# Optimization experiments

Hardware: AMD Instinct MI355X
Metric: run time of the kernel (lower is better)

The kernel has to match this reference:

```python
import jax, jax.numpy as jnp
import numpy as np

# Volume dims: 3 directional stacks, batch 1, 64 channels, (8,16,16) latent volume
STACK, B, C, D, H, W = 3, 1, 64, 8, 16, 16
S = D * H * W  # 2048 attention positions
NUM_HEADS = 8


def setup_inputs() -> dict:
    key = jax.random.key(0)
    kq, kk, kv = jax.random.split(key, 3)
    shape = (STACK, B, C, D, H, W)
    keys = jax.random.normal(kk, shape, dtype=jnp.float32)
    queries = jax.random.normal(kq, shape, dtype=jnp.float32)
    values = jax.random.normal(kv, shape, dtype=jnp.float32)
    # Causal (lower-triangular) mask over flattened spatial positions
    attn_mask = jnp.tril(jnp.ones((S, S), dtype=bool))
    return {"keys": keys, "queries": queries, "values": values,
            "attn_mask": attn_mask, "num_heads": NUM_HEADS}


def reference(keys, queries, values, attn_mask, num_heads):
    s, b, c, d, h, w = keys.shape
    nh = num_heads
    ck = c // nh            # channels per head (attention head dim)
    seq = d * h * w         # spatial positions = attention sequence length
    scale = ck ** (-0.5)
    # (s, b, nh, ck, seq)
    q = queries.reshape(s, b, nh, ck, seq) * scale
    k = keys.reshape(s, b, nh, ck, seq)
    v = values.reshape(s, b, nh, ck, seq)
    # logits[i, j] = <q[:, i], k[:, j]> over channel dim -> (s, b, nh, seq, seq)
    logits = jnp.einsum('sbhci,sbhcj->sbhij', q, k)
    # eval mode: dropout-on-logits trick is training-only, skipped here
    logits = jnp.where(attn_mask, logits, -jnp.inf)
    weights = jax.nn.softmax(logits, axis=-1)
    # (s, b, nh, seq, ck)
    attn = jnp.einsum('sbhij,sbhjc->sbhic', weights, jnp.swapaxes(v, 3, 4))
    # transpose back to channels-first, then restore spatial dims
    out = jnp.swapaxes(attn, 3, 4).reshape(s, b, nh * ck, d, h, w)
    return out
```

## Files before the change

### kernel.cpp

```cpp
#include <hip/hip_runtime.h>
#include <hip/hip_bf16.h>

constexpr int NPROB  = 24;
constexpr int SEQ    = 2048;
constexpr int CK     = 8;
constexpr int NSTRIP = SEQ / 16;

typedef __attribute__((ext_vector_type(8))) short bf16x8;
typedef __attribute__((ext_vector_type(4))) float f32x4;

__device__ constexpr float QSCALE = 0.35355339059327373f * 1.4426950408889634f;

__device__ inline unsigned packbf(float a, float b) {
    float2 t{a, b};
    __hip_bfloat162 h = __float22bfloat162_rn(t);
    unsigned r; __builtin_memcpy(&r, &h, 4); return r;
}

constexpr int T1 = NPROB * SEQ;
constexpr int T2 = NPROB * CK * (SEQ / 8);
constexpr int T3 = NPROB * 8  * (SEQ / 8);

__global__ __launch_bounds__(256) void prepass(
    const float* __restrict__ K, const float* __restrict__ Q,
    const float* __restrict__ V,
    uint4* __restrict__ Qt4, uint4* __restrict__ Kt4, uint4* __restrict__ V164)
{
    const int t = blockIdx.x * 256 + threadIdx.x;
    if (t < T1) {
        const int prob = t >> 11, j = t & (SEQ - 1);
        const float* qs = Q + prob * CK * SEQ + j;
        const float* ks = K + prob * CK * SEQ + j;
        uint4 qo, ko;
        qo.x = packbf(qs[0 * SEQ] * QSCALE, qs[1 * SEQ] * QSCALE);
        qo.y = packbf(qs[2 * SEQ] * QSCALE, qs[3 * SEQ] * QSCALE);
        qo.z = packbf(qs[4 * SEQ] * QSCALE, qs[5 * SEQ] * QSCALE);
        qo.w = packbf(qs[6 * SEQ] * QSCALE, qs[7 * SEQ] * QSCALE);
        ko.x = packbf(ks[0 * SEQ], ks[1 * SEQ]);
        ko.y = packbf(ks[2 * SEQ], ks[3 * SEQ]);
        ko.z = packbf(ks[4 * SEQ], ks[5 * SEQ]);
        ko.w = packbf(ks[6 * SEQ], ks[7 * SEQ]);
        Qt4[t] = qo;
        Kt4[t] = ko;
    } else if (t < T1 + T2) {
        const int idx  = t - T1;
        const int prob = idx >> 11;
        const int rem  = idx & 2047;
        const int c    = rem >> 8;
        const int u    = rem & 255;
        const int c32  = u >> 2;
        const int g    = u & 3;
        const float* vs = V + prob * CK * SEQ + c * SEQ + c32 * 32;
        const float4 a = *reinterpret_cast<const float4*>(vs + 4 * g);
        const float4 b = *reinterpret_cast<const float4*>(vs + 16 + 4 * g);
        uint4 vo;
        vo.x = packbf(a.x, a.y); vo.y = packbf(a.z, a.w);
        vo.z = packbf(b.x, b.y); vo.w = packbf(b.z, b.w);
        V164[prob * 4096 + c32 * 64 + g * 16 + c] = vo;
    } else {
        const int idx  = t - T1 - T2;
        const int prob = idx >> 11;
        const int rem  = idx & 2047;
        const int r    = rem >> 8;
        const int u    = rem & 255;
        const int c32  = u >> 2;
        const int g    = u & 3;
        const unsigned w = (r == 0) ? 0x3F803F80u : 0u;
        V164[prob * 4096 + c32 * 64 + g * 16 + (8 + r)] = uint4{w, w, w, w};
    }
}

__global__ __launch_bounds__(256) void attn_main(
    const uint4* __restrict__ Qt4, const uint4* __restrict__ Kt4,
    const uint4* __restrict__ V164, float* __restrict__ OUT)
{
    const int bid   = blockIdx.x;
    const int prob  = bid % NPROB;
    const int strip = (NSTRIP - 1) - (bid / NPROB);
    const int i0    = strip * 16;
    const int t  = threadIdx.x;
    const int w  = t >> 6;
    const int l  = t & 63;
    const int li = l & 15, g = l >> 4;

    const uint4* Ktp = Kt4 + prob * SEQ;
    const uint4* Vp  = V164 + prob * 4096;

    union { bf16x8 v; uint4 u; } qf;
    qf.u = (g == 0) ? Qt4[prob * SEQ + i0 + li] : uint4{0, 0, 0, 0};

    f32x4 acc = {0.f, 0.f, 0.f, 0.f};
    const f32x4 zc = {0.f, 0.f, 0.f, 0.f};
    const int mconst = li - 4 * g;

    const int NU = i0 >> 5;

#pragma unroll 2
    for (int p = w; p < NU; p += 4) {
        const int j0 = p * 32;
        union { bf16x8 v; uint4 u; } k0, k1, vf;
        k0.u = Ktp[j0 + li];
        k1.u = Ktp[j0 + 16 + li];
        vf.u = Vp[(p << 6) + l];
        f32x4 d0 = __builtin_amdgcn_mfma_f32_16x16x32_bf16(k0.v, qf.v, zc, 0, 0, 0);
        f32x4 d1 = __builtin_amdgcn_mfma_f32_16x16x32_bf16(k1.v, qf.v, zc, 0, 0, 0);
#pragma unroll
        for (int r = 0; r < 4; ++r) { d0[r] = exp2f(d0[r]); d1[r] = exp2f(d1[r]); }
        union { bf16x8 v; unsigned u[4]; } pa;
        pa.u[0] = packbf(d0[0], d0[1]);
        pa.u[1] = packbf(d0[2], d0[3]);
        pa.u[2] = packbf(d1[0], d1[1]);
        pa.u[3] = packbf(d1[2], d1[3]);
        acc = __builtin_amdgcn_mfma_f32_16x16x32_bf16(pa.v, vf.v, acc, 0, 0, 0);
    }

    if ((NU & 3) == w) {
        const int j0 = NU * 32;
        union { bf16x8 v; uint4 u; } k0, k1, vf;
        union { bf16x8 v; unsigned u[4]; } pa;
        vf.u = Vp[(NU << 6) + l];
        if (i0 & 16) {
            k0.u = Ktp[j0 + li];
            k1.u = Ktp[j0 + 16 + li];
            f32x4 d0 = __builtin_amdgcn_mfma_f32_16x16x32_bf16(k0.v, qf.v, zc, 0, 0, 0);
            f32x4 d1 = __builtin_amdgcn_mfma_f32_16x16x32_bf16(k1.v, qf.v, zc, 0, 0, 0);
#pragma unroll
            for (int r = 0; r < 4; ++r) {
                d0[r] = exp2f(d0[r]);
                d1[r] = (r <= mconst) ? exp2f(d1[r]) : 0.f;
            }
            pa.u[0] = packbf(d0[0], d0[1]);
            pa.u[1] = packbf(d0[2], d0[3]);
            pa.u[2] = packbf(d1[0], d1[1]);
            pa.u[3] = packbf(d1[2], d1[3]);
        } else {
            k0.u = Ktp[j0 + li];
            f32x4 d0 = __builtin_amdgcn_mfma_f32_16x16x32_bf16(k0.v, qf.v, zc, 0, 0, 0);
#pragma unroll
            for (int r = 0; r < 4; ++r)
                d0[r] = (r <= mconst) ? exp2f(d0[r]) : 0.f;
            pa.u[0] = packbf(d0[0], d0[1]);
            pa.u[1] = packbf(d0[2], d0[3]);
            pa.u[2] = 0u;
            pa.u[3] = 0u;
        }
        acc = __builtin_amdgcn_mfma_f32_16x16x32_bf16(pa.v, vf.v, acc, 0, 0, 0);
    }

    __shared__ f32x4 lds[4][64];
    lds[w][l] = acc;
    __syncthreads();
    if (w != 0) return;
#pragma unroll
    for (int ww = 1; ww < 4; ++ww) {
        const f32x4 o = lds[ww][l];
#pragma unroll
        for (int r = 0; r < 4; ++r) acc[r] += o[r];
    }

    const int idxR = ((g << 4) + 8) << 2;
    float inv[4];
#pragma unroll
    for (int r = 0; r < 4; ++r) {
        const float rs = __int_as_float(
            __builtin_amdgcn_ds_bpermute(idxR, __float_as_int(acc[r])));
        inv[r] = 1.0f / rs;
    }
    if (li < CK) {
#pragma unroll
        for (int r = 0; r < 4; ++r)
            OUT[(prob * CK + li) * SEQ + i0 + 4 * g + r] = acc[r] * inv[r];
    }
}

extern "C" void kernel_launch(void* const* d_in, const int* in_sizes, int n_in,
                              void* d_out, int out_size, void* d_ws, size_t ws_size,
                              hipStream_t stream) {
    const float* K = (const float*)d_in[0];
    const float* Q = (const float*)d_in[1];
    const float* V = (const float*)d_in[2];
    float* OUT = (float*)d_out;

    uint4* Qt4  = (uint4*)d_ws;
    uint4* Kt4  = (uint4*)((char*)d_ws + 786432);
    uint4* V164 = (uint4*)((char*)d_ws + 1572864);

    prepass<<<dim3((T1 + T2 + T3) / 256), dim3(256), 0, stream>>>(K, Q, V, Qt4, Kt4, V164);
    attn_main<<<dim3(NPROB * NSTRIP), dim3(256), 0, stream>>>(Qt4, Kt4, V164, OUT);
}
```

Before: 91.92 us.

## Process 64-query strips per block and convert Q inside attention kernel

Each block now handles four 16-row query tiles instead of one, so every K and V fragment loaded from global memory feeds four query tiles. The diagonal tile masking is generalized to per-tile thresholds. Q bf16 conversion and scaling moves out of the prepass into the main kernel, which removes a workspace write and read. The cost is fewer blocks (768 instead of 3072), so there is less parallelism and more load imbalance across the causal strips, plus higher register use per thread.

```diff
diff --git a/kernel.cpp b/kernel.cpp
--- a/kernel.cpp
+++ b/kernel.cpp
@@ -1,10 +1,10 @@
 #include <hip/hip_runtime.h>
 #include <hip/hip_bf16.h>
 
-constexpr int NPROB  = 24;
-constexpr int SEQ    = 2048;
-constexpr int CK     = 8;
-constexpr int NSTRIP = SEQ / 16;
+constexpr int NPROB   = 24;
+constexpr int SEQ     = 2048;
+constexpr int CK      = 8;
+constexpr int NSTRIP64 = SEQ / 64;
 
 typedef __attribute__((ext_vector_type(8))) short bf16x8;
 typedef __attribute__((ext_vector_type(4))) float f32x4;
@@ -17,33 +17,26 @@
     unsigned r; __builtin_memcpy(&r, &h, 4); return r;
 }
 
-constexpr int T1 = NPROB * SEQ;
-constexpr int T2 = NPROB * CK * (SEQ / 8);
-constexpr int T3 = NPROB * 8  * (SEQ / 8);
+constexpr int TK = NPROB * SEQ;
+constexpr int TB = NPROB * CK * (SEQ / 8);
+constexpr int TC = NPROB * 8  * (SEQ / 8);
 
 __global__ __launch_bounds__(256) void prepass(
-    const float* __restrict__ K, const float* __restrict__ Q,
-    const float* __restrict__ V,
-    uint4* __restrict__ Qt4, uint4* __restrict__ Kt4, uint4* __restrict__ V164)
+    const float* __restrict__ K, const float* __restrict__ V,
+    uint4* __restrict__ Kt4, uint4* __restrict__ V164)
 {
     const int t = blockIdx.x * 256 + threadIdx.x;
-    if (t < T1) {
+    if (t < TK) {
         const int prob = t >> 11, j = t & (SEQ - 1);
-        const float* qs = Q + prob * CK * SEQ + j;
         const float* ks = K + prob * CK * SEQ + j;
-        uint4 qo, ko;
-        qo.x = packbf(qs[0 * SEQ] * QSCALE, qs[1 * SEQ] * QSCALE);
-        qo.y = packbf(qs[2 * SEQ] * QSCALE, qs[3 * SEQ] * QSCALE);
-        qo.z = packbf(qs[4 * SEQ] * QSCALE, qs[5 * SEQ] * QSCALE);
-        qo.w = packbf(qs[6 * SEQ] * QSCALE, qs[7 * SEQ] * QSCALE);
+        uint4 ko;
         ko.x = packbf(ks[0 * SEQ], ks[1 * SEQ]);
         ko.y = packbf(ks[2 * SEQ], ks[3 * SEQ]);
         ko.z = packbf(ks[4 * SEQ], ks[5 * SEQ]);
         ko.w = packbf(ks[6 * SEQ], ks[7 * SEQ]);
-        Qt4[t] = qo;
         Kt4[t] = ko;
-    } else if (t < T1 + T2) {
-        const int idx  = t - T1;
+    } else if (t < TK + TB) {
+        const int idx  = t - TK;
         const int prob = idx >> 11;
         const int rem  = idx & 2047;
         const int c    = rem >> 8;
@@ -58,7 +51,7 @@
         vo.z = packbf(b.x, b.y); vo.w = packbf(b.z, b.w);
         V164[prob * 4096 + c32 * 64 + g * 16 + c] = vo;
     } else {
-        const int idx  = t - T1 - T2;
+        const int idx  = t - TK - TB;
         const int prob = idx >> 11;
         const int rem  = idx & 2047;
         const int r    = rem >> 8;
@@ -71,13 +64,13 @@
 }
 
 __global__ __launch_bounds__(256) void attn_main(
-    const uint4* __restrict__ Qt4, const uint4* __restrict__ Kt4,
+    const float* __restrict__ Q, const uint4* __restrict__ Kt4,
     const uint4* __restrict__ V164, float* __restrict__ OUT)
 {
-    const int bid   = blockIdx.x;
-    const int prob  = bid % NPROB;
-    const int strip = (NSTRIP - 1) - (bid / NPROB);
-    const int i0    = strip * 16;
+    const int bid  = blockIdx.x;
+    const int prob = bid % NPROB;
+    const int s64  = (NSTRIP64 - 1) - (bid / NPROB);
+    const int i0   = s64 * 64;
     const int t  = threadIdx.x;
     const int w  = t >> 6;
     const int l  = t & 63;
@@ -86,76 +79,81 @@
     const uint4* Ktp = Kt4 + prob * SEQ;
     const uint4* Vp  = V164 + prob * 4096;
 
-    union { bf16x8 v; uint4 u; } qf;
-    qf.u = (g == 0) ? Qt4[prob * SEQ + i0 + li] : uint4{0, 0, 0, 0};
-
-    f32x4 acc = {0.f, 0.f, 0.f, 0.f};
-    const f32x4 zc = {0.f, 0.f, 0.f, 0.f};
-    const int mconst = li - 4 * g;
-
-    const int NU = i0 >> 5;
-
-#pragma unroll 2
-    for (int p = w; p < NU; p += 4) {
-        const int j0 = p * 32;
-        union { bf16x8 v; uint4 u; } k0, k1, vf;
-        k0.u = Ktp[j0 + li];
-        k1.u = Ktp[j0 + 16 + li];
-        vf.u = Vp[(p << 6) + l];
-        f32x4 d0 = __builtin_amdgcn_mfma_f32_16x16x32_bf16(k0.v, qf.v, zc, 0, 0, 0);
-        f32x4 d1 = __builtin_amdgcn_mfma_f32_16x16x32_bf16(k1.v, qf.v, zc, 0, 0, 0);
+    const float* Qp = Q + prob * CK * SEQ;
+    union { bf16x8 v; uint4 u; } qf[4];
 #pragma unroll
-        for (int r = 0; r < 4; ++r) { d0[r] = exp2f(d0[r]); d1[r] = exp2f(d1[r]); }
-        union { bf16x8 v; unsigned u[4]; } pa;
-        pa.u[0] = packbf(d0[0], d0[1]);
-        pa.u[1] = packbf(d0[2], d0[3]);
-        pa.u[2] = packbf(d1[0], d1[1]);
-        pa.u[3] = packbf(d1[2], d1[3]);
-        acc = __builtin_amdgcn_mfma_f32_16x16x32_bf16(pa.v, vf.v, acc, 0, 0, 0);
+    for (int f = 0; f < 4; ++f) {
+        uint4 qo = {0u, 0u, 0u, 0u};
+        if (g == 0) {
+            const int qi = i0 + 16 * f + li;
+            qo.x = packbf(Qp[0 * SEQ + qi] * QSCALE, Qp[1 * SEQ + qi] * QSCALE);
+            qo.y = packbf(Qp[2 * SEQ + qi] * QSCALE, Qp[3 * SEQ + qi] * QSCALE);
+            qo.z = packbf(Qp[4 * SEQ + qi] * QSCALE, Qp[5 * SEQ + qi] * QSCALE);
+            qo.w = packbf(Qp[6 * SEQ + qi] * QSCALE, Qp[7 * SEQ + qi] * QSCALE);
+        }
+        qf[f].u = qo;
     }
 
-    if ((NU & 3) == w) {
-        const int j0 = NU * 32;
+    f32x4 acc[4];
+#pragma unroll
+    for (int f = 0; f < 4; ++f) acc[f] = f32x4{0.f, 0.f, 0.f, 0.f};
+    const f32x4 zc = {0.f, 0.f, 0.f, 0.f};
+
+    const int pint = 2 * s64;
+    const int pmax = 2 * s64 + 1;
+
+    for (int p = w; p <= pmax; p += 4) {
         union { bf16x8 v; uint4 u; } k0, k1, vf;
-        union { bf16x8 v; unsigned u[4]; } pa;
-        vf.u = Vp[(NU << 6) + l];
-        if (i0 & 16) {
-            k0.u = Ktp[j0 + li];
-            k1.u = Ktp[j0 + 16 + li];
-            f32x4 d0 = __builtin_amdgcn_mfma_f32_16x16x32_bf16(k0.v, qf.v, zc, 0, 0, 0);
-            f32x4 d1 = __builtin_amdgcn_mfma_f32_16x16x32_bf16(k1.v, qf.v, zc, 0, 0, 0);
+        k0.u = Ktp[p * 32 + li];
+        k1.u = Ktp[p * 32 + 16 + li];
+        vf.u = Vp[(p << 6) + l];
+        if (p < pint) {
 #pragma unroll
-            for (int r = 0; r < 4; ++r) {
-                d0[r] = exp2f(d0[r]);
-                d1[r] = (r <= mconst) ? exp2f(d1[r]) : 0.f;
+            for (int f = 0; f < 4; ++f) {
+                f32x4 d0 = __builtin_amdgcn_mfma_f32_16x16x32_bf16(k0.v, qf[f].v, zc, 0, 0, 0);
+                f32x4 d1 = __builtin_amdgcn_mfma_f32_16x16x32_bf16(k1.v, qf[f].v, zc, 0, 0, 0);
+#pragma unroll
+                for (int r = 0; r < 4; ++r) { d0[r] = exp2f(d0[r]); d1[r] = exp2f(d1[r]); }
+                union { bf16x8 v; unsigned u[4]; } pa;
+                pa.u[0] = packbf(d0[0], d0[1]);
+                pa.u[1] = packbf(d0[2], d0[3]);
+                pa.u[2] = packbf(d1[0], d1[1]);
+                pa.u[3] = packbf(d1[2], d1[3]);
+                acc[f] = __builtin_amdgcn_mfma_f32_16x16x32_bf16(pa.v, vf.v, acc[f], 0, 0, 0);
             }
-            pa.u[0] = packbf(d0[0], d0[1]);
-            pa.u[1] = packbf(d0[2], d0[3]);
-            pa.u[2] = packbf(d1[0], d1[1]);
-            pa.u[3] = packbf(d1[2], d1[3]);
         } else {
-            k0.u = Ktp[j0 + li];
-            f32x4 d0 = __builtin_amdgcn_mfma_f32_16x16x32_bf16(k0.v, qf.v, zc, 0, 0, 0);
 #pragma unroll
-            for (int r = 0; r < 4; ++r)
-                d0[r] = (r <= mconst) ? exp2f(d0[r]) : 0.f;
-            pa.u[0] = packbf(d0[0], d0[1]);
-            pa.u[1] = packbf(d0[2], d0[3]);
-            pa.u[2] = 0u;
-            pa.u[3] = 0u;
+            for (int f = 0; f < 4; ++f) {
+                const int thr0 = i0 + 16 * f + li - 32 * p - 4 * g;
+                const int thr1 = thr0 - 16;
+                f32x4 d0 = __builtin_amdgcn_mfma_f32_16x16x32_bf16(k0.v, qf[f].v, zc, 0, 0, 0);
+                f32x4 d1 = __builtin_amdgcn_mfma_f32_16x16x32_bf16(k1.v, qf[f].v, zc, 0, 0, 0);
+#pragma unroll
+                for (int r = 0; r < 4; ++r) {
+                    d0[r] = (r <= thr0) ? exp2f(d0[r]) : 0.f;
+                    d1[r] = (r <= thr1) ? exp2f(d1[r]) : 0.f;
+                }
+                union { bf16x8 v; unsigned u[4]; } pa;
+                pa.u[0] = packbf(d0[0], d0[1]);
+                pa.u[1] = packbf(d0[2], d0[3]);
+                pa.u[2] = packbf(d1[0], d1[1]);
+                pa.u[3] = packbf(d1[2], d1[3]);
+                acc[f] = __builtin_amdgcn_mfma_f32_16x16x32_bf16(pa.v, vf.v, acc[f], 0, 0, 0);
+            }
         }
-        acc = __builtin_amdgcn_mfma_f32_16x16x32_bf16(pa.v, vf.v, acc, 0, 0, 0);
     }
 
-    __shared__ f32x4 lds[4][64];
-    lds[w][l] = acc;
+    __shared__ f32x4 lds[4][4][64];
+#pragma unroll
+    for (int f = 0; f < 4; ++f) lds[w][f][l] = acc[f];
     __syncthreads();
-    if (w != 0) return;
+
+    f32x4 a = lds[0][w][l];
 #pragma unroll
     for (int ww = 1; ww < 4; ++ww) {
-        const f32x4 o = lds[ww][l];
+        const f32x4 o = lds[ww][w][l];
 #pragma unroll
-        for (int r = 0; r < 4; ++r) acc[r] += o[r];
+        for (int r = 0; r < 4; ++r) a[r] += o[r];
     }
 
     const int idxR = ((g << 4) + 8) << 2;
@@ -163,13 +161,13 @@
 #pragma unroll
     for (int r = 0; r < 4; ++r) {
         const float rs = __int_as_float(
-            __builtin_amdgcn_ds_bpermute(idxR, __float_as_int(acc[r])));
+            __builtin_amdgcn_ds_bpermute(idxR, __float_as_int(a[r])));
         inv[r] = 1.0f / rs;
     }
     if (li < CK) {
 #pragma unroll
         for (int r = 0; r < 4; ++r)
-            OUT[(prob * CK + li) * SEQ + i0 + 4 * g + r] = acc[r] * inv[r];
+            OUT[(prob * CK + li) * SEQ + i0 + 16 * w + 4 * g + r] = a[r] * inv[r];
     }
 }
 
@@ -181,10 +179,9 @@
     const float* V = (const float*)d_in[2];
     float* OUT = (float*)d_out;
 
-    uint4* Qt4  = (uint4*)d_ws;
-    uint4* Kt4  = (uint4*)((char*)d_ws + 786432);
-    uint4* V164 = (uint4*)((char*)d_ws + 1572864);
+    uint4* Kt4  = (uint4*)d_ws;
+    uint4* V164 = (uint4*)((char*)d_ws + 786432);
 
-    prepass<<<dim3((T1 + T2 + T3) / 256), dim3(256), 0, stream>>>(K, Q, V, Qt4, Kt4, V164);
-    attn_main<<<dim3(NPROB * NSTRIP), dim3(256), 0, stream>>>(Qt4, Kt4, V164, OUT);
+    prepass<<<dim3((TK + TB + TC) / 256), dim3(256), 0, stream>>>(K, V, Kt4, V164);
+    attn_main<<<dim3(NPROB * NSTRIP64), dim3(256), 0, stream>>>(Q, Kt4, V164, OUT);
 }
```

New measurement: 98.02 us. 1.07x slower.
